# Performance work log

Measured on AMD Instinct MI355X. Metric: run time of the kernel, lower is better.

The kernel has to match this reference:

```python
import jax, jax.numpy as jnp
import numpy as np

B, N, K = 8, 2048, 8
NEG_SLOPE = 0.2
EPS = 1e-5


def lrelu(x):
    return jax.nn.leaky_relu(x, NEG_SLOPE)


def bn(x, axes):
    # BatchNorm forward with batch statistics, affine at init (gamma=1, beta=0)
    m = x.mean(axes, keepdims=True)
    v = x.var(axes, keepdims=True)
    return (x - m) / jnp.sqrt(v + EPS)


def knn(x, k):
    # x: [B, C, N] -> idx [B, N, K] of nearest neighbors (incl. self), as in DGCNN
    xx = jnp.sum(x * x, axis=1)                      # [B, N]
    inner = jnp.einsum('bcn,bcm->bnm', x, x)         # [B, N, N]
    pair = -(xx[:, :, None] - 2.0 * inner + xx[:, None, :])  # -||xi-xj||^2
    return jax.lax.top_k(pair, k)[1]                 # [B, N, K]


def get_graph_feature(x, idx):
    # x: [B, C, N], idx: [B, N, K] -> [B, 2C, N, K] = cat(neighbor-center, center)
    nb = jax.vmap(lambda xb, ib: xb[:, ib])(x, idx)  # [B, C, N, K]
    ctr = x[:, :, :, None]
    return jnp.concatenate([nb - ctr, jnp.broadcast_to(ctr, nb.shape)], axis=1)


def edge_block(e, W):
    # 1x1 conv2d (no bias) + BN2d + LeakyReLU on [B, C, N, K]
    h = jnp.einsum('oc,bcnk->bonk', W, e)
    return lrelu(bn(h, (0, 2, 3)))


def setup_inputs() -> dict:
    key = jax.random.key(0)
    ks = jax.random.split(key, 10)
    def w(k, shape):
        fan_in = shape[-1]
        return jax.random.normal(k, shape, jnp.float32) / np.sqrt(fan_in)
    return {
        'x': jax.random.normal(ks[0], (B, N, 3), jnp.float32),
        'start_neighs': jax.random.randint(ks[1], (B, N, K), 0, N, jnp.int32),
        'u_noise': jax.random.uniform(ks[2], (B, 70, N), jnp.float32, 1e-6, 1.0 - 1e-6),
        'W0': w(ks[3], (64, 6)),
        'W1': w(ks[4], (128, 128)),
        'W2': w(ks[5], (256, 256)),
        'W3': w(ks[6], (512, 512)),
        'W4': w(ks[7], (1024, 960)),
        'Wm1': w(ks[8], (512, 1024)),
        'Wm2': w(ks[9], (70, 512)),
    }


def reference(x, start_neighs, u_noise, W0, W1, W2, W3, W4, Wm1, Wm2):
    xt = jnp.swapaxes(x, 1, 2)                        # [B, 3, N]
    # EdgeConv 0: uses provided start_neighs
    e = get_graph_feature(xt, start_neighs)           # [B, 6, N, K]
    h = edge_block(e, W0)                             # [B, 64, N, K]
    outs = [h.max(axis=-1)]                           # [B, 64, N]
    # EdgeConvs 1..3: dynamic knn on current features (only_true_neighs=False)
    for W in (W1, W2, W3):
        prev = outs[-1]
        idx = knn(prev, K)
        e = get_graph_feature(prev, idx)              # [B, 2C, N, K]
        h = edge_block(e, W)
        outs.append(h.max(axis=-1))
    cat = jnp.concatenate(outs, axis=1)               # [B, 960, N]
    feat = lrelu(bn(jnp.einsum('oc,bcn->bon', W4, cat), (0, 2)))  # [B, 1024, N]
    # masking prediction head
    hm = lrelu(bn(jnp.einsum('oc,bcn->bon', Wm1, feat), (0, 2)))  # [B, 512, N]
    logits = jnp.einsum('oc,bcn->bon', Wm2, hm)       # [B, 70, N]
    # gumbel softmax (tau=1, hard=True) over last dim (points), straight-through
    g = -jnp.log(-jnp.log(u_noise))
    soft = jax.nn.softmax(logits + g, axis=-1)
    hard = jax.nn.one_hot(jnp.argmax(soft, axis=-1), N, dtype=soft.dtype)
    y = hard + soft - jax.lax.stop_gradient(soft)     # values are exactly 0/1
    return jnp.transpose(y, (1, 0, 2))[..., None]     # [70, B, N, 1]
```

## Files before the change

### kernel.cpp

```cpp
#include <hip/hip_runtime.h>
#include <math.h>

#define Bsz 8
#define Nsz 2048
#define Ksz 8
#define NSLOPE 0.2f
#define EPSV 1e-5f
#define LOSCALE 2048.0f
#define INV_LOSCALE (1.0f / 2048.0f)

typedef _Float16 half8 __attribute__((ext_vector_type(8)));
typedef float floatx4 __attribute__((ext_vector_type(4)));

__device__ __forceinline__ int swzk(int k, int row)
{
    return (k & ~31) | ((((k >> 3) + (row >> 1)) & 3) << 3) | (k & 7);
}

__device__ __forceinline__ void glds16(const _Float16* g, _Float16* l)
{
    __builtin_amdgcn_global_load_lds(
        (const __attribute__((address_space(1))) unsigned int*)g,
        (__attribute__((address_space(3))) unsigned int*)l, 16, 0, 0);
}

__device__ __forceinline__ void split2(float v, _Float16& h, _Float16& l)
{
    _Float16 hh = (_Float16)v;
    h = hh;
    l = (_Float16)((v - (float)hh) * LOSCALE);
}

template <int EPI>
__launch_bounds__(512) __global__
void hgemm_k(const _Float16* __restrict__ Ahi, const _Float16* __restrict__ Alo,
             long long sAb, int lda,
             const _Float16* __restrict__ Bhi, const _Float16* __restrict__ Blo,
             long long sBb, int ldb,
             float* __restrict__ C, long long sCb, int ldc,
             int Mreal, int Kk, const float* __restrict__ xx)
{
    __shared__ _Float16 sm[16384];
    const int b = blockIdx.z;
    const int m0 = blockIdx.y * 128, n0 = blockIdx.x * 128;
    const int tid = threadIdx.x;
    const int w = tid >> 6, lane = tid & 63;
    const int quad = lane >> 4, r16 = lane & 15;
    const int wm = (w >> 1) * 32, wn = (w & 1) * 64;
    const int sq = (r16 >> 1) & 3;
    const int kchunk = ((quad + sq) & 3) * 8;

    const _Float16* Ah = Ahi + (long long)b * sAb;
    const _Float16* Al = Alo + (long long)b * sAb;
    const _Float16* Bh = Bhi + (long long)b * sBb;
    const _Float16* Bl = Blo + (long long)b * sBb;

    floatx4 acc_h[2][4], acc_m[2][4];
#pragma unroll
    for (int i = 0; i < 2; i++)
#pragma unroll
        for (int j = 0; j < 4; j++) {
            acc_h[i][j] = (floatx4){0.f, 0.f, 0.f, 0.f};
            acc_m[i][j] = (floatx4){0.f, 0.f, 0.f, 0.f};
        }

    const int srow = tid >> 2;
    const int sseg = (tid & 3) * 8;

    for (int k0 = 0; k0 < Kk; k0 += 32) {
        long long aoff = (long long)(m0 + srow) * lda + k0 + sseg;
        long long boff = (long long)(n0 + srow) * ldb + k0 + sseg;
        glds16(Ah + aoff, &sm[tid * 8]);
        glds16(Al + aoff, &sm[4096 + tid * 8]);
        glds16(Bh + boff, &sm[8192 + tid * 8]);
        glds16(Bl + boff, &sm[12288 + tid * 8]);
        __syncthreads();

        half8 ah[2], al[2];
#pragma unroll
        for (int i = 0; i < 2; i++) {
            int off = (wm + i * 16 + r16) * 32 + kchunk;
            ah[i] = *(const half8*)&sm[off];
            al[i] = *(const half8*)&sm[4096 + off];
        }
#pragma unroll
        for (int j = 0; j < 4; j++) {
            int off = (wn + j * 16 + r16) * 32 + kchunk;
            half8 bh = *(const half8*)&sm[8192 + off];
            half8 bl = *(const half8*)&sm[12288 + off];
#pragma unroll
            for (int i = 0; i < 2; i++) {
                acc_h[i][j] = __builtin_amdgcn_mfma_f32_16x16x32_f16(ah[i], bh, acc_h[i][j], 0, 0, 0);
                acc_m[i][j] = __builtin_amdgcn_mfma_f32_16x16x32_f16(ah[i], bl, acc_m[i][j], 0, 0, 0);
                acc_m[i][j] = __builtin_amdgcn_mfma_f32_16x16x32_f16(al[i], bh, acc_m[i][j], 0, 0, 0);
            }
        }
        __syncthreads();
    }

    float* Cb = C + (long long)b * sCb;
    const float* xxp = EPI ? (xx + (long long)b * Nsz) : xx;
#pragma unroll
    for (int i = 0; i < 2; i++) {
#pragma unroll
        for (int r = 0; r < 4; r++) {
            int gm = m0 + wm + i * 16 + quad * 4 + r;
            if (gm >= Mreal) continue;
            float xm = EPI ? xxp[gm] : 0.f;
#pragma unroll
            for (int j = 0; j < 4; j++) {
                int gn = n0 + wn + j * 16 + r16;
                float v = acc_h[i][j][r] + acc_m[i][j][r] * INV_LOSCALE;
                if (EPI == 1) v = -((xm - 2.f * v) + xxp[gn]);
                Cb[(long long)gm * ldc + gn] = v;
            }
        }
    }
}

__launch_bounds__(256) __global__
void topk8_thresh_k(const float* __restrict__ pair, int* __restrict__ idxo)
{
    const int lane = threadIdx.x & 63;
    const int row = blockIdx.x * 4 + (threadIdx.x >> 6);
    const float* pr = pair + (size_t)row * Nsz;

    unsigned vals[32];
#pragma unroll
    for (int c = 0; c < 32; c++) {
        unsigned u = __float_as_uint(pr[c * 64 + lane]);
        vals[c] = (u & 0x80000000u) ? ~u : (u | 0x80000000u);
    }

    unsigned t[8] = {0, 0, 0, 0, 0, 0, 0, 0};
#pragma unroll
    for (int c = 0; c < 32; c++) {
        unsigned key = vals[c];
#pragma unroll
        for (int j = 7; j >= 1; --j) {
            unsigned m = t[j - 1] < key ? t[j - 1] : key;
            t[j] = t[j] > m ? t[j] : m;
        }
        t[0] = t[0] > key ? t[0] : key;
    }
#pragma unroll
    for (int d = 1; d < 64; d <<= 1) {
        unsigned oth[8];
#pragma unroll
        for (int j = 0; j < 8; j++) oth[j] = __shfl_xor(t[j], d, 64);
        unsigned c2[8];
#pragma unroll
        for (int j = 0; j < 8; j++) {
            unsigned a = t[j], b2 = oth[7 - j];
            c2[j] = a > b2 ? a : b2;
        }
#define CE(A, B) { unsigned x = c2[A], y = c2[B]; c2[A] = x > y ? x : y; c2[B] = x > y ? y : x; }
        CE(0, 4) CE(1, 5) CE(2, 6) CE(3, 7)
        CE(0, 2) CE(1, 3) CE(4, 6) CE(5, 7)
        CE(0, 1) CE(2, 3) CE(4, 5) CE(6, 7)
#undef CE
#pragma unroll
        for (int j = 0; j < 8; j++) t[j] = c2[j];
    }
    const unsigned T = t[7];

    const unsigned long long lmask = (1ull << lane) - 1ull;
    int* op = idxo + (size_t)row * 8;
    int g = 0;
#pragma unroll
    for (int c = 0; c < 32; c++) {
        unsigned long long m = __ballot(vals[c] > T);
        if (vals[c] > T) op[g + __popcll(m & lmask)] = c * 64 + lane;
        g += __popcll(m);
    }
    const int needed = 8 - g;
    int e = 0;
    for (int c = 0; c < 32; c++) {
        if (e >= needed) break;
        unsigned long long m = __ballot(vals[c] == T);
        int pos = e + __popcll(m & lmask);
        if (vals[c] == T && pos < needed) op[g + pos] = c * 64 + lane;
        e += __popcll(m);
    }
}

__launch_bounds__(256) __global__
void sgemm_k(const float* __restrict__ A, int lda,
             const float* __restrict__ Bm, long long sBb, int ldb,
             float* __restrict__ C, long long sCb, int ldc,
             int M, int Kk)
{
    __shared__ float As[16][64];
    __shared__ float Bs[16][64];
    const int b = blockIdx.z;
    const float* Bb = Bm + (long long)b * sBb;
    const int m0 = blockIdx.y * 64, n0 = blockIdx.x * 64;
    const int tid = threadIdx.x;
    const int am = tid >> 2, ak = (tid & 3) * 4;
    const int bk = tid >> 6, bn = tid & 63;
    const int tx = tid & 15, ty = tid >> 4;
    float acc[4][4] = {};
    for (int k0 = 0; k0 < Kk; k0 += 16) {
#pragma unroll
        for (int i = 0; i < 4; i++) {
            int gk = k0 + ak + i;
            int gm = m0 + am;
            As[ak + i][am] = (gk < Kk && gm < M) ? A[(long long)gm * lda + gk] : 0.f;
        }
#pragma unroll
        for (int i = 0; i < 4; i++) {
            int kk = bk + i * 4;
            int gk = k0 + kk;
            Bs[kk][bn] = (gk < Kk) ? Bb[(long long)gk * ldb + (n0 + bn)] : 0.f;
        }
        __syncthreads();
#pragma unroll
        for (int kk = 0; kk < 16; kk++) {
            float a[4], bb2[4];
#pragma unroll
            for (int i = 0; i < 4; i++) a[i] = As[kk][ty * 4 + i];
#pragma unroll
            for (int j = 0; j < 4; j++) bb2[j] = Bs[kk][tx * 4 + j];
#pragma unroll
            for (int i = 0; i < 4; i++)
#pragma unroll
                for (int j = 0; j < 4; j++)
                    acc[i][j] = fmaf(a[i], bb2[j], acc[i][j]);
        }
        __syncthreads();
    }
    float* Cb = C + (long long)b * sCb;
#pragma unroll
    for (int i = 0; i < 4; i++) {
        int gm = m0 + ty * 4 + i;
        if (gm >= M) continue;
#pragma unroll
        for (int j = 0; j < 4; j++)
            Cb[(long long)gm * ldc + n0 + tx * 4 + j] = acc[i][j];
    }
}

#define T0 16384
#define T1 (T0 + 192)
#define T2 (T1 + 16384)
#define T3 (T2 + 65536)
#define T4 (T3 + 262144)
#define T5 (T4 + 983040)
#define T6 (T5 + 524288)
#define T7 (T6 + 65536)
#define WOFF_E1 0
#define WOFF_E2 16384
#define WOFF_E3 81920
#define WOFF_W4 344064
#define WOFF_M1 1327104
#define WOFF_M2 1851392

__device__ __forceinline__ void split_plain(const float* W, _Float16* wh, _Float16* wl,
                                            size_t base, int t, int M, int Kk)
{
    int oo = t / Kk, c = t - oo * Kk;
    float v = (oo < M) ? W[(size_t)oo * Kk + c] : 0.f;
    _Float16 h, l;
    split2(v, h, l);
    size_t d = base + (size_t)oo * Kk + swzk(c, oo);
    wh[d] = h; wl[d] = l;
}

__device__ __forceinline__ void split_edge(const float* W, _Float16* wh, _Float16* wl,
                                           size_t base, int t, int O, int C)
{
    int oo = t / C, c = t - oo * C;
    float v;
    if (oo < O) v = W[(size_t)oo * 2 * C + c];
    else { int o2 = oo - O; v = W[(size_t)o2 * 2 * C + C + c] - W[(size_t)o2 * 2 * C + c]; }
    _Float16 h, l;
    split2(v, h, l);
    size_t d = base + (size_t)oo * C + swzk(c, oo);
    wh[d] = h; wl[d] = l;
}

__global__ void mega_prep_k(const float* __restrict__ x,
                            const float* __restrict__ W0, const float* __restrict__ W1,
                            const float* __restrict__ W2, const float* __restrict__ W3,
                            const float* __restrict__ W4, const float* __restrict__ Wm1,
                            const float* __restrict__ Wm2,
                            float* __restrict__ xt, float* __restrict__ wcat32,
                            _Float16* __restrict__ wh, _Float16* __restrict__ wl)
{
    int t = blockIdx.x * 256 + threadIdx.x;
    if (t < T0) {
        int n = t & (Nsz - 1), b = t >> 11;
#pragma unroll
        for (int c = 0; c < 3; c++)
            xt[((size_t)b * 3 + c) * Nsz + n] = x[((size_t)b * Nsz + n) * 3 + c];
    } else if (t < T1) {
        int u = t - T0;
        int oo = u / 3, c = u % 3;
        float a = W0[(size_t)oo * 6 + c];
        float b2 = W0[(size_t)oo * 6 + 3 + c];
        wcat32[(size_t)oo * 3 + c] = a;
        wcat32[(size_t)(64 + oo) * 3 + c] = b2 - a;
    } else if (t < T2) {
        split_edge(W1, wh, wl, WOFF_E1, t - T1, 128, 64);
    } else if (t < T3) {
        split_edge(W2, wh, wl, WOFF_E2, t - T2, 256, 128);
    } else if (t < T4) {
        split_edge(W3, wh, wl, WOFF_E3, t - T3, 512, 256);
    } else if (t < T5) {
        split_plain(W4, wh, wl, WOFF_W4, t - T4, 1024, 960);
    } else if (t < T6) {
        split_plain(Wm1, wh, wl, WOFF_M1, t - T5, 512, 1024);
    } else if (t < T7) {
        split_plain(Wm2, wh, wl, WOFF_M2, t - T6, 70, 512);
    }
}

__global__ void xx_planes_k(const _Float16* __restrict__ catA, const _Float16* __restrict__ catB,
                            float* __restrict__ xx, int off, int C)
{
    int t = blockIdx.x * 256 + threadIdx.x;
    if (t >= Bsz * Nsz) return;
    int n = t & (Nsz - 1), b = t >> 11;
    size_t base = ((size_t)b * Nsz + n) * 1024 + off;
    float s = 0.f;
    for (int c8 = 0; c8 < C / 8; c8++) {
        half8 h = *(const half8*)&catA[base + c8 * 8];
        half8 l = *(const half8*)&catB[base + c8 * 8];
#pragma unroll
        for (int e = 0; e < 8; e++) {
            float vh = (float)h[e];
            float vl = (float)l[e] * INV_LOSCALE;
            s = fmaf(vh, vh, s);
            s = fmaf(2.f * vh, vl, s);
        }
    }
    xx[t] = s;
}

__global__ void gather_pool_t_k(const float* __restrict__ R, const int* __restrict__ idx,
                                _Float16* __restrict__ catA, _Float16* __restrict__ catB,
                                float* __restrict__ part, int O, int off)
{
    __shared__ float tile[64][65];
    const int tid = threadIdx.x;
    const int lane = tid & 63, w = tid >> 6;
    const int n0 = blockIdx.x * 64, o0 = blockIdx.y * 64, b = blockIdx.z;
    const int n = n0 + lane;

    int id[8];
    {
        const int* ip = idx + ((size_t)b * Nsz + n) * 8;
#pragma unroll
        for (int k = 0; k < 8; k++) id[k] = ip[k];
    }
    const float* Rb = R + (size_t)b * 2 * O * Nsz;
#pragma unroll
    for (int i = 0; i < 16; i++) {
        int o_l = w + i * 4;
        int o = o0 + o_l;
        const float* P = Rb + (size_t)o * Nsz;
        float q = Rb[(size_t)(O + o) * Nsz + n];
        float hmax = -INFINITY, s1 = 0.f, s2 = 0.f;
#pragma unroll
        for (int k = 0; k < 8; k++) {
            float h = P[id[k]] + q;
            hmax = fmaxf(hmax, h);
            s1 += h;
            s2 += h * h;
        }
        tile[o_l][lane] = hmax;
#pragma unroll
        for (int offs = 32; offs; offs >>= 1) {
            s1 += __shfl_xor(s1, offs, 64);
            s2 += __shfl_xor(s2, offs, 64);
        }
        if (lane == 0) {
            size_t pi = ((size_t)o * Bsz + b) * 32 + blockIdx.x;
            part[pi * 2] = s1;
            part[pi * 2 + 1] = s2;
        }
    }
    __syncthreads();
    int n_l = tid >> 2, quad = tid & 3;
    int nrow = n0 + n_l;
    half8 h0, h1, l0, l1;
#pragma unroll
    for (int e = 0; e < 8; e++) {
        _Float16 hh, ll;
        split2(tile[quad * 16 + e][n_l], hh, ll);
        h0[e] = hh; l0[e] = ll;
        split2(tile[quad * 16 + 8 + e][n_l], hh, ll);
        h1[e] = hh; l1[e] = ll;
    }
    size_t rowb = ((size_t)b * Nsz + nrow) * 1024;
    int c0 = off + o0 + quad * 16;
    *(half8*)&catA[rowb + swzk(c0, nrow)] = h0;
    *(half8*)&catA[rowb + swzk(c0 + 8, nrow)] = h1;
    *(half8*)&catB[rowb + swzk(c0, nrow)] = l0;
    *(half8*)&catB[rowb + swzk(c0 + 8, nrow)] = l1;
}

__global__ void stats_reduce_k(const float* __restrict__ part, float* __restrict__ stats)
{
    int o2 = blockIdx.x;
    int t = threadIdx.x;
    float s1 = part[((size_t)o2 * 256 + t) * 2];
    float s2 = part[((size_t)o2 * 256 + t) * 2 + 1];
#pragma unroll
    for (int off = 32; off; off >>= 1) { s1 += __shfl_xor(s1, off, 64); s2 += __shfl_xor(s2, off, 64); }
    __shared__ float sh[8];
    int w = t >> 6;
    if ((t & 63) == 0) { sh[w] = s1; sh[4 + w] = s2; }
    __syncthreads();
    if (t == 0) {
        stats[2 * o2] = sh[0] + sh[1] + sh[2] + sh[3];
        stats[2 * o2 + 1] = sh[4] + sh[5] + sh[6] + sh[7];
    }
}

__global__ void fc_stats_k(const float* __restrict__ buf, float* __restrict__ stats, int O)
{
    int oo = blockIdx.x;
    int t = threadIdx.x;
    float s1 = 0.f, s2 = 0.f;
    for (int i = t; i < Bsz * Nsz; i += 256) {
        int b = i >> 11, n = i & (Nsz - 1);
        float v = buf[((size_t)b * O + oo) * Nsz + n];
        s1 += v; s2 += v * v;
    }
#pragma unroll
    for (int off = 32; off; off >>= 1) { s1 += __shfl_xor(s1, off, 64); s2 += __shfl_xor(s2, off, 64); }
    __shared__ float sh[8];
    int w = t >> 6;
    if ((t & 63) == 0) { sh[w] = s1; sh[4 + w] = s2; }
    __syncthreads();
    if (t == 0) {
        stats[2 * oo] = sh[0] + sh[1] + sh[2] + sh[3];
        stats[2 * oo + 1] = sh[4] + sh[5] + sh[6] + sh[7];
    }
}

__global__ void bn_t_k(_Float16* __restrict__ catA, _Float16* __restrict__ catB,
                       const float* __restrict__ stats, int off, int O, float invCnt)
{
    int per_n = O / 8;
    size_t t = (size_t)blockIdx.x * 256 + threadIdx.x;
    if (t >= (size_t)Bsz * Nsz * per_n) return;
    int c8 = (int)(t % per_n);
    size_t rest = t / per_n;
    int n = (int)(rest & (Nsz - 1));
    int b = (int)(rest >> 11);
    size_t base = ((size_t)b * Nsz + n) * 1024 + off + c8 * 8;
    int oo_base = ((c8 >> 2) << 5) + ((((c8 & 3) - (n >> 1)) & 3) << 3);
    half8 h = *(const half8*)&catA[base];
    half8 l = *(const half8*)&catB[base];
    half8 ho, lo;
#pragma unroll
    for (int e = 0; e < 8; e++) {
        int oo = oo_base + e;
        float mean = stats[2 * oo] * invCnt;
        float var = stats[2 * oo + 1] * invCnt - mean * mean;
        float v = (float)h[e] + (float)l[e] * INV_LOSCALE;
        float z = (v - mean) / sqrtf(var + EPSV);
        z = z >= 0.f ? z : NSLOPE * z;
        _Float16 hh, ll;
        split2(z, hh, ll);
        ho[e] = hh; lo[e] = ll;
    }
    *(half8*)&catA[base] = ho;
    *(half8*)&catB[base] = lo;
}

__global__ void bn_split_t_k(const float* __restrict__ src, const float* __restrict__ stats,
                             _Float16* __restrict__ dA, _Float16* __restrict__ dB,
                             int O, int ldt, float invCnt)
{
    __shared__ float tile[64][65];
    const int tid = threadIdx.x;
    const int n0 = blockIdx.x * 64, o0 = blockIdx.y * 64, b = blockIdx.z;
#pragma unroll
    for (int i = 0; i < 16; i++) {
        int flat = tid + 256 * i;
        int o_l = flat >> 6, n_l = flat & 63;
        int oo = o0 + o_l;
        float mean = stats[2 * oo] * invCnt;
        float var = stats[2 * oo + 1] * invCnt - mean * mean;
        float v = src[((size_t)b * O + oo) * Nsz + n0 + n_l];
        float z = (v - mean) / sqrtf(var + EPSV);
        tile[o_l][n_l] = z >= 0.f ? z : NSLOPE * z;
    }
    __syncthreads();
    int n_l = tid >> 2, quad = tid & 3;
    int nrow = n0 + n_l;
    half8 h0, h1, l0, l1;
#pragma unroll
    for (int e = 0; e < 8; e++) {
        _Float16 hh, ll;
        split2(tile[quad * 16 + e][n_l], hh, ll);
        h0[e] = hh; l0[e] = ll;
        split2(tile[quad * 16 + 8 + e][n_l], hh, ll);
        h1[e] = hh; l1[e] = ll;
    }
    size_t rowb = ((size_t)b * Nsz + nrow) * ldt;
    int c0 = o0 + quad * 16;
    *(half8*)&dA[rowb + swzk(c0, nrow)] = h0;
    *(half8*)&dA[rowb + swzk(c0 + 8, nrow)] = h1;
    *(half8*)&dB[rowb + swzk(c0, nrow)] = l0;
    *(half8*)&dB[rowb + swzk(c0 + 8, nrow)] = l1;
}

__global__ void gumbel_onehot_k(const float* __restrict__ logits, const float* __restrict__ u,
                                float* __restrict__ out)
{
    int lane = threadIdx.x & 63;
    int wv = threadIdx.x >> 6;
    int row = blockIdx.x * 4 + wv;
    int b = row / 70, oo = row % 70;
    const float* L = logits + (size_t)row * Nsz;
    const float* U = u + (size_t)row * Nsz;
    float bv = -INFINITY; int bi = 0x7fffffff;
    for (int n = lane; n < Nsz; n += 64) {
        float g = -logf(-logf(U[n]));
        float z = L[n] + g;
        if (z > bv) { bv = z; bi = n; }
    }
#pragma unroll
    for (int off = 32; off; off >>= 1) {
        float ov = __shfl_xor(bv, off, 64);
        int oi = __shfl_xor(bi, off, 64);
        if (ov > bv || (ov == bv && oi < bi)) { bv = ov; bi = oi; }
    }
    float* Or = out + ((size_t)oo * Bsz + b) * Nsz;
    for (int n = lane; n < Nsz; n += 64) Or[n] = (n == bi) ? 1.f : 0.f;
}

extern "C" void kernel_launch(void* const* d_in, const int* in_sizes, int n_in,
                              void* d_out, int out_size, void* d_ws, size_t ws_size,
                              hipStream_t stream)
{
    (void)in_sizes; (void)n_in; (void)out_size; (void)ws_size;
    const float* x   = (const float*)d_in[0];
    const int*   sn  = (const int*)d_in[1];
    const float* un  = (const float*)d_in[2];
    const float* W0  = (const float*)d_in[3];
    const float* W1  = (const float*)d_in[4];
    const float* W2  = (const float*)d_in[5];
    const float* W3  = (const float*)d_in[6];
    const float* W4  = (const float*)d_in[7];
    const float* Wm1 = (const float*)d_in[8];
    const float* Wm2 = (const float*)d_in[9];
    float* out = (float*)d_out;

    char* ws = (char*)d_ws;
    size_t o = 0;
    _Float16* catA = (_Float16*)(ws + o); o += (size_t)Bsz * Nsz * 1024 * 2;
    _Float16* catB = (_Float16*)(ws + o); o += (size_t)Bsz * Nsz * 1024 * 2;
    float* R       = (float*)(ws + o);    o += (size_t)Bsz * 1024 * Nsz * 4;
    _Float16* wHi  = (_Float16*)(ws + o); o += (size_t)2 * 1024 * 1024 * 2;
    _Float16* wLo  = (_Float16*)(ws + o); o += (size_t)2 * 1024 * 1024 * 2;
    float* xt      = (float*)(ws + o);    o += (size_t)Bsz * 3 * Nsz * 4;
    float* xxb     = (float*)(ws + o);    o += (size_t)Bsz * Nsz * 4;
    float* wcat32  = (float*)(ws + o);    o += 4096;
    float* part    = (float*)(ws + o);    o += (size_t)512 * Bsz * 32 * 2 * 4;
    float* stats   = (float*)(ws + o);    o += 2048 * 4;
    int* idxb      = (int*)(ws + o);      o += (size_t)Bsz * Nsz * Ksz * 4;
    float* logits  = R + (size_t)12 * 1024 * 1024;

    const long long catStride = (long long)Nsz * 1024;

    mega_prep_k<<<(T7 + 255) / 256, 256, 0, stream>>>(x, W0, W1, W2, W3, W4, Wm1, Wm2,
                                                      xt, wcat32, wHi, wLo);

    sgemm_k<<<dim3(32, 2, Bsz), 256, 0, stream>>>(wcat32, 3, xt, 3LL * Nsz, Nsz,
                                                  R, 2LL * 64 * Nsz, Nsz, 128, 3);
    gather_pool_t_k<<<dim3(32, 1, Bsz), 256, 0, stream>>>(R, sn, catA, catB, part, 64, 0);
    stats_reduce_k<<<64, 256, 0, stream>>>(part, stats);
    bn_t_k<<<(int)(((size_t)Bsz * Nsz * 8 + 255) / 256), 256, 0, stream>>>(
        catA, catB, stats, 0, 64, 1.f / 131072.f);

    struct LayerDesc { int C; int O; int prevOff; int catOff; size_t woff; };
    LayerDesc L[3] = {
        { 64, 128, 0, 64, WOFF_E1 },
        { 128, 256, 64, 192, WOFF_E2 },
        { 256, 512, 192, 448, WOFF_E3 },
    };
    for (int li = 0; li < 3; li++) {
        int C = L[li].C, O = L[li].O;
        int poff = L[li].prevOff;
        xx_planes_k<<<(Bsz * Nsz + 255) / 256, 256, 0, stream>>>(catA, catB, xxb, poff, C);
        for (int ch = 0; ch < 2; ch++) {
            const _Float16* pA = catA + poff + (size_t)ch * 4 * catStride;
            const _Float16* pB = catB + poff + (size_t)ch * 4 * catStride;
            hgemm_k<1><<<dim3(16, 16, 4), 512, 0, stream>>>(
                pA, pB, catStride, 1024, pA, pB, catStride, 1024,
                R, (long long)Nsz * Nsz, Nsz, Nsz, C, xxb + (size_t)ch * 4 * Nsz);
            topk8_thresh_k<<<4 * Nsz / 4, 256, 0, stream>>>(R, idxb + (size_t)ch * 4 * Nsz * Ksz);
        }
        hgemm_k<0><<<dim3(16, 2 * O / 128, Bsz), 512, 0, stream>>>(
            wHi + L[li].woff, wLo + L[li].woff, 0, C, catA + poff, catB + poff, catStride, 1024,
            R, 2LL * O * Nsz, Nsz, 2 * O, C, nullptr);
        gather_pool_t_k<<<dim3(32, O / 64, Bsz), 256, 0, stream>>>(
            R, idxb, catA, catB, part, O, L[li].catOff);
        stats_reduce_k<<<O, 256, 0, stream>>>(part, stats);
        bn_t_k<<<(int)(((size_t)Bsz * Nsz * (O / 8) + 255) / 256), 256, 0, stream>>>(
            catA, catB, stats, L[li].catOff, O, 1.f / 131072.f);
    }

    hgemm_k<0><<<dim3(16, 8, Bsz), 512, 0, stream>>>(
        wHi + WOFF_W4, wLo + WOFF_W4, 0, 960, catA, catB, catStride, 1024,
        R, 1024LL * Nsz, Nsz, 1024, 960, nullptr);
    fc_stats_k<<<1024, 256, 0, stream>>>(R, stats, 1024);
    bn_split_t_k<<<dim3(32, 16, Bsz), 256, 0, stream>>>(R, stats, catA, catB, 1024, 1024,
                                                        1.f / 16384.f);
    hgemm_k<0><<<dim3(16, 4, Bsz), 512, 0, stream>>>(
        wHi + WOFF_M1, wLo + WOFF_M1, 0, 1024, catA, catB, catStride, 1024,
        R, 512LL * Nsz, Nsz, 512, 1024, nullptr);
    fc_stats_k<<<512, 256, 0, stream>>>(R, stats, 512);
    bn_split_t_k<<<dim3(32, 8, Bsz), 256, 0, stream>>>(R, stats, catA, catB, 512, 512,
                                                       1.f / 16384.f);
    hgemm_k<0><<<dim3(16, 1, Bsz), 512, 0, stream>>>(
        wHi + WOFF_M2, wLo + WOFF_M2, 0, 512, catA, catB, (long long)Nsz * 512, 512,
        logits, 70LL * Nsz, Nsz, 70, 512, nullptr);

    gumbel_onehot_k<<<(Bsz * 70) / 4, 256, 0, stream>>>(logits, un, out);
}
```

Baseline: 934.4 us.

## Fuse kNN distance GEMM with per-tile top-8 selection and merge candidates

Replaces the full N×N pairwise-distance matrix write plus a separate row-wise top-8 kernel with a fused GEMM that selects the top-8 per 128-column tile directly from LDS. The 16 per-tile candidate lists are then merged in a small second kernel using 64-bit keys that pack value and index. This removes the large distance-matrix round-trip to global memory and the two-chunk batching. In exchange it adds extra syncs and LDS staging in the GEMM epilogue, and the merge kernel reduces 64-bit values across lanes with shuffles.

```diff
diff --git a/kernel.cpp b/kernel.cpp
--- a/kernel.cpp
+++ b/kernel.cpp
@@ -29,6 +29,21 @@
     _Float16 hh = (_Float16)v;
     h = hh;
     l = (_Float16)((v - (float)hh) * LOSCALE);
+}
+
+__device__ __forceinline__ unsigned long long shfl_xor64(unsigned long long x, int off)
+{
+    unsigned lo = __shfl_xor((unsigned)x, off, 64);
+    unsigned hi = __shfl_xor((unsigned)(x >> 32), off, 64);
+    return ((unsigned long long)hi << 32) | lo;
+}
+
+__device__ __forceinline__ void ins8_64(unsigned long long (&t)[8], unsigned long long key)
+{
+#pragma unroll
+    for (int j = 7; j >= 1; --j)
+        t[j] = (key > t[j - 1]) ? t[j - 1] : ((key > t[j]) ? key : t[j]);
+    t[0] = (key > t[0]) ? key : t[0];
 }
 
 template <int EPI>
@@ -118,69 +133,187 @@
     }
 }
 
-__launch_bounds__(256) __global__
-void topk8_thresh_k(const float* __restrict__ pair, int* __restrict__ idxo)
-{
-    const int lane = threadIdx.x & 63;
-    const int row = blockIdx.x * 4 + (threadIdx.x >> 6);
-    const float* pr = pair + (size_t)row * Nsz;
-
-    unsigned vals[32];
-#pragma unroll
-    for (int c = 0; c < 32; c++) {
-        unsigned u = __float_as_uint(pr[c * 64 + lane]);
-        vals[c] = (u & 0x80000000u) ? ~u : (u | 0x80000000u);
-    }
-
-    unsigned t[8] = {0, 0, 0, 0, 0, 0, 0, 0};
-#pragma unroll
-    for (int c = 0; c < 32; c++) {
-        unsigned key = vals[c];
-#pragma unroll
-        for (int j = 7; j >= 1; --j) {
-            unsigned m = t[j - 1] < key ? t[j - 1] : key;
-            t[j] = t[j] > m ? t[j] : m;
-        }
-        t[0] = t[0] > key ? t[0] : key;
-    }
-#pragma unroll
-    for (int d = 1; d < 64; d <<= 1) {
-        unsigned oth[8];
-#pragma unroll
-        for (int j = 0; j < 8; j++) oth[j] = __shfl_xor(t[j], d, 64);
-        unsigned c2[8];
-#pragma unroll
-        for (int j = 0; j < 8; j++) {
-            unsigned a = t[j], b2 = oth[7 - j];
-            c2[j] = a > b2 ? a : b2;
-        }
+__launch_bounds__(512) __global__
+void hgemm_cand_k(const _Float16* __restrict__ Phi, const _Float16* __restrict__ Plo,
+                  long long sPb, int ldp,
+                  unsigned long long* __restrict__ cand,
+                  int Kk, const float* __restrict__ xx)
+{
+    __shared__ float smf[64 * 129];
+    _Float16* sm = (_Float16*)smf;
+    const int b = blockIdx.z;
+    const int m0 = blockIdx.y * 128, n0 = blockIdx.x * 128;
+    const int tid = threadIdx.x;
+    const int w = tid >> 6, lane = tid & 63;
+    const int quad = lane >> 4, r16 = lane & 15;
+    const int wm = (w >> 1) * 32, wn = (w & 1) * 64;
+    const int sq = (r16 >> 1) & 3;
+    const int kchunk = ((quad + sq) & 3) * 8;
+
+    const _Float16* Ah = Phi + (long long)b * sPb;
+    const _Float16* Al = Plo + (long long)b * sPb;
+
+    floatx4 acc_h[2][4], acc_m[2][4];
+#pragma unroll
+    for (int i = 0; i < 2; i++)
+#pragma unroll
+        for (int j = 0; j < 4; j++) {
+            acc_h[i][j] = (floatx4){0.f, 0.f, 0.f, 0.f};
+            acc_m[i][j] = (floatx4){0.f, 0.f, 0.f, 0.f};
+        }
+
+    const int srow = tid >> 2;
+    const int sseg = (tid & 3) * 8;
+
+    for (int k0 = 0; k0 < Kk; k0 += 32) {
+        long long aoff = (long long)(m0 + srow) * ldp + k0 + sseg;
+        long long boff = (long long)(n0 + srow) * ldp + k0 + sseg;
+        glds16(Ah + aoff, &sm[tid * 8]);
+        glds16(Al + aoff, &sm[4096 + tid * 8]);
+        glds16(Ah + boff, &sm[8192 + tid * 8]);
+        glds16(Al + boff, &sm[12288 + tid * 8]);
+        __syncthreads();
+
+        half8 ah[2], al[2];
+#pragma unroll
+        for (int i = 0; i < 2; i++) {
+            int off = (wm + i * 16 + r16) * 32 + kchunk;
+            ah[i] = *(const half8*)&sm[off];
+            al[i] = *(const half8*)&sm[4096 + off];
+        }
+#pragma unroll
+        for (int j = 0; j < 4; j++) {
+            int off = (wn + j * 16 + r16) * 32 + kchunk;
+            half8 bh = *(const half8*)&sm[8192 + off];
+            half8 bl = *(const half8*)&sm[12288 + off];
+#pragma unroll
+            for (int i = 0; i < 2; i++) {
+                acc_h[i][j] = __builtin_amdgcn_mfma_f32_16x16x32_f16(ah[i], bh, acc_h[i][j], 0, 0, 0);
+                acc_m[i][j] = __builtin_amdgcn_mfma_f32_16x16x32_f16(ah[i], bl, acc_m[i][j], 0, 0, 0);
+                acc_m[i][j] = __builtin_amdgcn_mfma_f32_16x16x32_f16(al[i], bh, acc_m[i][j], 0, 0, 0);
+            }
+        }
+        __syncthreads();
+    }
+
+    const float* xxp = xx + (long long)b * Nsz;
+    const int row8 = tid >> 3;
+    const int s8 = tid & 7;
+    const int gshift = (lane >> 3) * 8;
+
+#pragma unroll
+    for (int p = 0; p < 2; p++) {
+        __syncthreads();
+        if ((w >> 2) == p) {
+            int rbase = wm - p * 64;
+#pragma unroll
+            for (int i = 0; i < 2; i++) {
+#pragma unroll
+                for (int r = 0; r < 4; r++) {
+                    int row_l = rbase + i * 16 + quad * 4 + r;
+                    float xm = xxp[m0 + p * 64 + row_l];
+#pragma unroll
+                    for (int j = 0; j < 4; j++) {
+                        int col = wn + j * 16 + r16;
+                        float a = acc_h[i][j][r] + acc_m[i][j][r] * INV_LOSCALE;
+                        smf[row_l * 129 + col] = -((xm - 2.f * a) + xxp[n0 + col]);
+                    }
+                }
+            }
+        }
+        __syncthreads();
+
+        unsigned vals[16];
+#pragma unroll
+        for (int c = 0; c < 16; c++) {
+            unsigned u = __float_as_uint(smf[row8 * 129 + s8 + c * 8]);
+            vals[c] = (u & 0x80000000u) ? ~u : (u | 0x80000000u);
+        }
+        unsigned t[8] = {0, 0, 0, 0, 0, 0, 0, 0};
+#pragma unroll
+        for (int c = 0; c < 16; c++) {
+            unsigned key = vals[c];
+#pragma unroll
+            for (int j = 7; j >= 1; --j) {
+                unsigned m = t[j - 1] < key ? t[j - 1] : key;
+                t[j] = t[j] > m ? t[j] : m;
+            }
+            t[0] = t[0] > key ? t[0] : key;
+        }
+#pragma unroll
+        for (int d = 1; d < 8; d <<= 1) {
+            unsigned oth[8];
+#pragma unroll
+            for (int j = 0; j < 8; j++) oth[j] = __shfl_xor(t[j], d, 64);
+            unsigned c2[8];
+#pragma unroll
+            for (int j = 0; j < 8; j++) {
+                unsigned a = t[j], b2 = oth[7 - j];
+                c2[j] = a > b2 ? a : b2;
+            }
 #define CE(A, B) { unsigned x = c2[A], y = c2[B]; c2[A] = x > y ? x : y; c2[B] = x > y ? y : x; }
-        CE(0, 4) CE(1, 5) CE(2, 6) CE(3, 7)
-        CE(0, 2) CE(1, 3) CE(4, 6) CE(5, 7)
-        CE(0, 1) CE(2, 3) CE(4, 5) CE(6, 7)
+            CE(0, 4) CE(1, 5) CE(2, 6) CE(3, 7)
+            CE(0, 2) CE(1, 3) CE(4, 6) CE(5, 7)
+            CE(0, 1) CE(2, 3) CE(4, 5) CE(6, 7)
 #undef CE
 #pragma unroll
-        for (int j = 0; j < 8; j++) t[j] = c2[j];
-    }
-    const unsigned T = t[7];
-
-    const unsigned long long lmask = (1ull << lane) - 1ull;
+            for (int j = 0; j < 8; j++) t[j] = c2[j];
+        }
+        const unsigned T = t[7];
+
+        int gm = m0 + p * 64 + row8;
+        unsigned long long* cp = cand + (((size_t)b * Nsz + gm) * 16 + blockIdx.x) * 8;
+        const unsigned smask = (1u << s8) - 1u;
+        int g = 0;
+#pragma unroll
+        for (int c = 0; c < 16; c++) {
+            unsigned long long m = __ballot(vals[c] > T);
+            unsigned byte = (unsigned)(m >> gshift) & 0xFFu;
+            if (vals[c] > T) {
+                int pos = g + __popc(byte & smask);
+                int gn = n0 + s8 + c * 8;
+                cp[pos] = ((unsigned long long)vals[c] << 32) | (0xFFFFFFFFu - (unsigned)gn);
+            }
+            g += __popc(byte);
+        }
+        const int needed = 8 - g;
+        int e = 0;
+        for (int c = 0; c < 16 && e < needed; c++) {
+            unsigned long long m = __ballot(vals[c] == T);
+            unsigned byte = (unsigned)(m >> gshift) & 0xFFu;
+            int pos = e + __popc(byte & smask);
+            if (vals[c] == T && pos < needed) {
+                int gn = n0 + s8 + c * 8;
+                cp[g + pos] = ((unsigned long long)T << 32) | (0xFFFFFFFFu - (unsigned)gn);
+            }
+            e += __popc(byte);
+        }
+    }
+}
+
+__global__ void merge_cand_k(const unsigned long long* __restrict__ cand,
+                             int* __restrict__ idxo)
+{
+    int lane = threadIdx.x & 63;
+    int row = blockIdx.x * 4 + (threadIdx.x >> 6);
+    const unsigned long long* cr = cand + (size_t)row * 128;
+    unsigned long long t[8] = {0, 0, 0, 0, 0, 0, 0, 0};
+    ins8_64(t, cr[lane]);
+    ins8_64(t, cr[lane + 64]);
     int* op = idxo + (size_t)row * 8;
-    int g = 0;
-#pragma unroll
-    for (int c = 0; c < 32; c++) {
-        unsigned long long m = __ballot(vals[c] > T);
-        if (vals[c] > T) op[g + __popcll(m & lmask)] = c * 64 + lane;
-        g += __popcll(m);
-    }
-    const int needed = 8 - g;
-    int e = 0;
-    for (int c = 0; c < 32; c++) {
-        if (e >= needed) break;
-        unsigned long long m = __ballot(vals[c] == T);
-        int pos = e + __popcll(m & lmask);
-        if (vals[c] == T && pos < needed) op[g + pos] = c * 64 + lane;
-        e += __popcll(m);
+#pragma unroll
+    for (int r = 0; r < 8; r++) {
+        unsigned long long best = t[0];
+#pragma unroll
+        for (int off = 32; off; off >>= 1) {
+            unsigned long long o = shfl_xor64(best, off);
+            if (o > best) best = o;
+        }
+        bool own = (t[0] == best);
+#pragma unroll
+        for (int j = 0; j < 7; j++) t[j] = own ? t[j + 1] : t[j];
+        t[7] = own ? 0ull : t[7];
+        if (lane == 0) op[r] = (int)(0xFFFFFFFFu - (unsigned)(best & 0xFFFFFFFFull));
     }
 }
 
@@ -564,6 +697,7 @@
     float* part    = (float*)(ws + o);    o += (size_t)512 * Bsz * 32 * 2 * 4;
     float* stats   = (float*)(ws + o);    o += 2048 * 4;
     int* idxb      = (int*)(ws + o);      o += (size_t)Bsz * Nsz * Ksz * 4;
+    unsigned long long* cand = (unsigned long long*)R;
     float* logits  = R + (size_t)12 * 1024 * 1024;
 
     const long long catStride = (long long)Nsz * 1024;
@@ -588,14 +722,9 @@
         int C = L[li].C, O = L[li].O;
         int poff = L[li].prevOff;
         xx_planes_k<<<(Bsz * Nsz + 255) / 256, 256, 0, stream>>>(catA, catB, xxb, poff, C);
-        for (int ch = 0; ch < 2; ch++) {
-            const _Float16* pA = catA + poff + (size_t)ch * 4 * catStride;
-            const _Float16* pB = catB + poff + (size_t)ch * 4 * catStride;
-            hgemm_k<1><<<dim3(16, 16, 4), 512, 0, stream>>>(
-                pA, pB, catStride, 1024, pA, pB, catStride, 1024,
-                R, (long long)Nsz * Nsz, Nsz, Nsz, C, xxb + (size_t)ch * 4 * Nsz);
-            topk8_thresh_k<<<4 * Nsz / 4, 256, 0, stream>>>(R, idxb + (size_t)ch * 4 * Nsz * Ksz);
-        }
+        hgemm_cand_k<<<dim3(16, 16, Bsz), 512, 0, stream>>>(
+            catA + poff, catB + poff, catStride, 1024, cand, C, xxb);
+        merge_cand_k<<<Bsz * Nsz / 4, 256, 0, stream>>>(cand, idxb);
         hgemm_k<0><<<dim3(16, 2 * O / 128, Bsz), 512, 0, stream>>>(
             wHi + L[li].woff, wLo + L[li].woff, 0, C, catA + poff, catB + poff, catStride, 1024,
             R, 2LL * O * Nsz, Nsz, 2 * O, C, nullptr);
```

New measurement: 955.6 us. 1.02x slower.
